# Optimization experiments

Hardware: AMD Instinct MI355X
Metric: run time of the kernel (lower is better)

The kernel has to match this reference:

```python
import jax, jax.numpy as jnp
import numpy as np

N_NODES = 100000
N_EDGES = 1600000
NFEAT = 256
NHID = 128


def setup_inputs() -> dict:
    key = jax.random.key(0)
    ks = jax.random.split(key, 8)
    x = jax.random.normal(ks[0], (N_NODES, NFEAT), dtype=jnp.float32)
    edge_row = jax.random.randint(ks[1], (N_EDGES,), 0, N_NODES, dtype=jnp.int32)
    edge_col = jax.random.randint(ks[2], (N_EDGES,), 0, N_NODES, dtype=jnp.int32)
    edge_val = jax.random.uniform(ks[3], (N_EDGES,), dtype=jnp.float32)
    # Glorot-ish init for the two GraphConvolution weights
    W1 = jax.random.normal(ks[4], (NFEAT, NHID), dtype=jnp.float32) * (1.0 / np.sqrt(NFEAT))
    b1 = jnp.zeros((NHID,), dtype=jnp.float32)
    W2 = jax.random.normal(ks[5], (NHID, NHID), dtype=jnp.float32) * (1.0 / np.sqrt(NHID))
    b2 = jnp.zeros((NHID,), dtype=jnp.float32)
    return {"x": x, "edge_row": edge_row, "edge_col": edge_col,
            "edge_val": edge_val, "W1": W1, "b1": b1, "W2": W2, "b2": b2}


def _gcn_layer(h, W, b, edge_row, edge_col, edge_val, n_nodes):
    # support = h @ W  (dense transform), then spmm(adj, support) + b
    support = h @ W                              # [N, d_out]
    msgs = edge_val[:, None] * support[edge_col]  # [E, d_out] gather
    agg = jax.ops.segment_sum(msgs, edge_row, num_segments=n_nodes)  # scatter-add
    return agg + b


def reference(x, edge_row, edge_col, edge_val, W1, b1, W2, b2):
    n = x.shape[0]
    # eval mode: dropout is identity
    h = jax.nn.relu(_gcn_layer(x, W1, b1, edge_row, edge_col, edge_val, n))
    for _ in range(4):  # gc2 applied 4 times with shared weights
        h = jax.nn.relu(_gcn_layer(h, W2, b2, edge_row, edge_col, edge_val, n))
    return h
```

## Files before the change

### kernel.cpp

```cpp
#include <hip/hip_runtime.h>

constexpr int NFEAT = 256;
constexpr int NHID  = 128;
constexpr int SCAN_B = 4096;


__global__ void hist_kernel(const int* __restrict__ rows, int* __restrict__ cnt, int n) {
  int i = blockIdx.x * blockDim.x + threadIdx.x;
  if (i < n) atomicAdd(&cnt[rows[i]], 1);
}

__global__ void scan1_kernel(const int* __restrict__ cnt, int* __restrict__ part,
                             int* __restrict__ bsum, int n) {
  __shared__ int tmp[1024];
  int tid = threadIdx.x;
  int base = blockIdx.x * SCAN_B + tid * 4;
  int4 v = make_int4(0, 0, 0, 0);
  if (base + 4 <= n) {
    v = *(const int4*)&cnt[base];
  } else {
    if (base + 0 < n) v.x = cnt[base + 0];
    if (base + 1 < n) v.y = cnt[base + 1];
    if (base + 2 < n) v.z = cnt[base + 2];
    if (base + 3 < n) v.w = cnt[base + 3];
  }
  int s = v.x + v.y + v.z + v.w;
  tmp[tid] = s;
  __syncthreads();
  for (int off = 1; off < 1024; off <<= 1) {
    int t = (tid >= off) ? tmp[tid - off] : 0;
    __syncthreads();
    tmp[tid] += t;
    __syncthreads();
  }
  int excl = tmp[tid] - s;
  if (base + 0 < n) part[base + 0] = excl;
  if (base + 1 < n) part[base + 1] = excl + v.x;
  if (base + 2 < n) part[base + 2] = excl + v.x + v.y;
  if (base + 3 < n) part[base + 3] = excl + v.x + v.y + v.z;
  if (tid == 1023) bsum[blockIdx.x] = tmp[1023];
}

__global__ void scan2_kernel(int* __restrict__ bsum, int nb) {
  if (threadIdx.x == 0 && blockIdx.x == 0) {
    int run = 0;
    for (int i = 0; i < nb; ++i) { int t = bsum[i]; bsum[i] = run; run += t; }
    bsum[nb] = run;
  }
}

__global__ void scan3_kernel(int* __restrict__ row_ptr, const int* __restrict__ bsum,
                             int* __restrict__ cursor, int n, int nb) {
  int i = blockIdx.x * blockDim.x + threadIdx.x;
  if (i < n) {
    int v = row_ptr[i] + bsum[i / SCAN_B];
    row_ptr[i] = v;
    cursor[i]  = v;
  }
  if (i == 0) row_ptr[n] = bsum[nb];
}

__global__ void scatter_kernel(const int* __restrict__ rows, const int* __restrict__ cols,
                               const float* __restrict__ vals, int* __restrict__ cursor,
                               int2* __restrict__ ev_s, int n) {
  int i = blockIdx.x * blockDim.x + threadIdx.x;
  if (i < n) {
    int p = atomicAdd(&cursor[rows[i]], 1);
    ev_s[p] = make_int2(cols[i], __float_as_int(vals[i]));
  }
}


__device__ __forceinline__ void gload16(const float* src, float* dst_lds) {
  __builtin_amdgcn_global_load_lds(
      (const __attribute__((address_space(1))) void*)src,
      (__attribute__((address_space(3))) void*)dst_lds,
      16, 0, 0);
}

template<int K>
__global__ __launch_bounds__(256, 4) void gemm_kernel(const float* __restrict__ A,
                                                      const float* __restrict__ W,
                                                      float* __restrict__ C, int M) {
  __shared__ __align__(16) float As[2][2048];
  __shared__ __align__(16) float Bs[2][2048];
  const int tid  = threadIdx.x;
  const int w    = tid >> 6;
  const int lane = tid & 63;
  const int r8   = tid >> 4;
  const int c8   = tid & 15;
  const int block_row = blockIdx.x * 128;

  float acc[2][2][4][4] = {};

  auto prefetch = [&](int t) {
    const int buf = t & 1;
    const int k0  = t * 16;
    #pragma unroll
    for (int j = 0; j < 2; ++j) {
      int s   = j * 256 + w * 64 + lane;
      int row = s >> 2;
      int q   = (s & 3) ^ ((row >> 2) & 3);
      int grow = block_row + row;
      if (grow >= M) grow = M - 1;
      gload16(A + (size_t)grow * K + k0 + q * 4,
              &As[buf][(j * 256 + w * 64) * 4]);
    }
    #pragma unroll
    for (int j = 0; j < 2; ++j) {
      int s = j * 256 + w * 64 + lane;
      int r = s >> 5, cq = s & 31;
      gload16(W + (size_t)(k0 + r) * 128 + cq * 4,
              &Bs[buf][(j * 256 + w * 64) * 4]);
    }
  };

  constexpr int NT = K / 16;
  prefetch(0);
  for (int t = 0; t < NT; ++t) {
    __syncthreads();
    if (t + 1 < NT) prefetch(t + 1);
    const float* as = As[t & 1];
    const float* bs = Bs[t & 1];
    #pragma unroll
    for (int q = 0; q < 4; ++q) {
      float4 b[4][2];
      #pragma unroll
      for (int j = 0; j < 4; ++j) {
        int kk = q * 4 + j;
        b[j][0] = *(const float4*)&bs[(kk * 32 + c8) * 4];
        b[j][1] = *(const float4*)&bs[(kk * 32 + 16 + c8) * 4];
      }
      #pragma unroll
      for (int rh = 0; rh < 2; ++rh)
        #pragma unroll
        for (int i = 0; i < 4; ++i) {
          int row = rh * 64 + r8 * 4 + i;
          float4 a = *(const float4*)&as[(row * 4 + (q ^ ((row >> 2) & 3))) * 4];
          float av[4] = {a.x, a.y, a.z, a.w};
          #pragma unroll
          for (int j = 0; j < 4; ++j)
            #pragma unroll
            for (int ch = 0; ch < 2; ++ch) {
              acc[rh][ch][i][0] += av[j] * b[j][ch].x;
              acc[rh][ch][i][1] += av[j] * b[j][ch].y;
              acc[rh][ch][i][2] += av[j] * b[j][ch].z;
              acc[rh][ch][i][3] += av[j] * b[j][ch].w;
            }
        }
    }
  }

  #pragma unroll
  for (int rh = 0; rh < 2; ++rh)
    #pragma unroll
    for (int i = 0; i < 4; ++i) {
      int grow = block_row + rh * 64 + r8 * 4 + i;
      if (grow < M) {
        #pragma unroll
        for (int ch = 0; ch < 2; ++ch) {
          float4 v = make_float4(acc[rh][ch][i][0], acc[rh][ch][i][1],
                                 acc[rh][ch][i][2], acc[rh][ch][i][3]);
          *(float4*)&C[(size_t)grow * 128 + ch * 64 + c8 * 4] = v;
        }
      }
    }
}


__global__ void spmm_kernel(const float* __restrict__ support, const int* __restrict__ row_ptr,
                            const int2* __restrict__ ev, const float* __restrict__ bias,
                            float* __restrict__ out, int n_nodes) {
  int row  = blockIdx.x * (blockDim.x >> 6) + (threadIdx.x >> 6);
  int lane = threadIdx.x & 63;
  if (row >= n_nodes) return;
  int beg = row_ptr[row], end = row_ptr[row + 1];
  float ax0 = 0.f, ay0 = 0.f, ax1 = 0.f, ay1 = 0.f;
  for (int chunk = beg; chunk < end; chunk += 64) {
    int idx = chunk + lane;
    int m = min(64, end - chunk);
    int2 ee = (idx < end) ? ev[idx] : make_int2(0, 0);
    int cl = ee.x;
    float vl = __int_as_float(ee.y);
    int e = 0;
    for (; e + 8 <= m; e += 8) {
      int   c0 = __shfl(cl, e + 0), c1 = __shfl(cl, e + 1);
      int   c2 = __shfl(cl, e + 2), c3 = __shfl(cl, e + 3);
      int   c4 = __shfl(cl, e + 4), c5 = __shfl(cl, e + 5);
      int   c6 = __shfl(cl, e + 6), c7 = __shfl(cl, e + 7);
      float v0 = __shfl(vl, e + 0), v1 = __shfl(vl, e + 1);
      float v2 = __shfl(vl, e + 2), v3 = __shfl(vl, e + 3);
      float v4 = __shfl(vl, e + 4), v5 = __shfl(vl, e + 5);
      float v6 = __shfl(vl, e + 6), v7 = __shfl(vl, e + 7);
      float2 s0 = *(const float2*)&support[(size_t)c0 * 128 + lane * 2];
      float2 s1 = *(const float2*)&support[(size_t)c1 * 128 + lane * 2];
      float2 s2 = *(const float2*)&support[(size_t)c2 * 128 + lane * 2];
      float2 s3 = *(const float2*)&support[(size_t)c3 * 128 + lane * 2];
      float2 s4 = *(const float2*)&support[(size_t)c4 * 128 + lane * 2];
      float2 s5 = *(const float2*)&support[(size_t)c5 * 128 + lane * 2];
      float2 s6 = *(const float2*)&support[(size_t)c6 * 128 + lane * 2];
      float2 s7 = *(const float2*)&support[(size_t)c7 * 128 + lane * 2];
      ax0 += v0 * s0.x; ay0 += v0 * s0.y;
      ax1 += v1 * s1.x; ay1 += v1 * s1.y;
      ax0 += v2 * s2.x; ay0 += v2 * s2.y;
      ax1 += v3 * s3.x; ay1 += v3 * s3.y;
      ax0 += v4 * s4.x; ay0 += v4 * s4.y;
      ax1 += v5 * s5.x; ay1 += v5 * s5.y;
      ax0 += v6 * s6.x; ay0 += v6 * s6.y;
      ax1 += v7 * s7.x; ay1 += v7 * s7.y;
    }
    for (; e < m; ++e) {
      int   ce = __shfl(cl, e);
      float ve = __shfl(vl, e);
      float2 s = *(const float2*)&support[(size_t)ce * 128 + lane * 2];
      ax0 += ve * s.x; ay0 += ve * s.y;
    }
  }
  float accx = ax0 + ax1, accy = ay0 + ay1;
  float2 b = *(const float2*)&bias[lane * 2];
  float2 o = make_float2(fmaxf(accx + b.x, 0.f), fmaxf(accy + b.y, 0.f));
  *(float2*)&out[(size_t)row * 128 + lane * 2] = o;
}


extern "C" void kernel_launch(void* const* d_in, const int* in_sizes, int n_in,
                              void* d_out, int out_size, void* d_ws, size_t ws_size,
                              hipStream_t stream) {
  const float* x    = (const float*)d_in[0];
  const int*   erow = (const int*)d_in[1];
  const int*   ecol = (const int*)d_in[2];
  const float* evl  = (const float*)d_in[3];
  const float* W1   = (const float*)d_in[4];
  const float* b1   = (const float*)d_in[5];
  const float* W2   = (const float*)d_in[6];
  const float* b2   = (const float*)d_in[7];
  int n_nodes = in_sizes[0] / NFEAT;
  int n_edges = in_sizes[1];
  float* out = (float*)d_out;

  char* ws = (char*)d_ws;
  size_t off = 0;
  auto alloc = [&](size_t bytes) -> void* {
    void* p = ws + off;
    off += bytes;
    off = (off + 255) & ~(size_t)255;
    return p;
  };
  float* support = (float*)alloc((size_t)n_nodes * NHID * sizeof(float));
  int*   cnt     = (int*)alloc((size_t)n_nodes * sizeof(int));
  int*   row_ptr = (int*)alloc(((size_t)n_nodes + 1) * sizeof(int));
  int*   cursor  = (int*)alloc((size_t)n_nodes * sizeof(int));
  int2*  ev_s    = (int2*)alloc((size_t)n_edges * sizeof(int2));
  int nb = (n_nodes + SCAN_B - 1) / SCAN_B;
  int*   bsum    = (int*)alloc((size_t)(nb + 1) * sizeof(int));

  hipMemsetAsync(cnt, 0, (size_t)n_nodes * sizeof(int), stream);
  hist_kernel<<<(n_edges + 255) / 256, 256, 0, stream>>>(erow, cnt, n_edges);
  scan1_kernel<<<nb, 1024, 0, stream>>>(cnt, row_ptr, bsum, n_nodes);
  scan2_kernel<<<1, 64, 0, stream>>>(bsum, nb);
  scan3_kernel<<<(n_nodes + 255) / 256, 256, 0, stream>>>(row_ptr, bsum, cursor, n_nodes, nb);
  scatter_kernel<<<(n_edges + 255) / 256, 256, 0, stream>>>(erow, ecol, evl, cursor,
                                                            ev_s, n_edges);

  int gblocks = (n_nodes + 127) / 128;
  int sblocks = (n_nodes + 3) / 4;

  gemm_kernel<NFEAT><<<gblocks, 256, 0, stream>>>(x, W1, support, n_nodes);
  spmm_kernel<<<sblocks, 256, 0, stream>>>(support, row_ptr, ev_s, b1, out, n_nodes);

  for (int l = 0; l < 4; ++l) {
    gemm_kernel<NHID><<<gblocks, 256, 0, stream>>>(out, W2, support, n_nodes);
    spmm_kernel<<<sblocks, 256, 0, stream>>>(support, row_ptr, ev_s, b2, out, n_nodes);
  }
}
```

Measured before the change: 1.081 ms.

## Store edge permutation instead of packed sorted edges; reorder GEMM inner loop

The scatter step now writes only a permutation index per edge instead of a packed (col, val) pair. Each SpMM then reads the permutation and gathers col and val from the original unsorted edge arrays. The GEMM inner loop is reordered to load all A values first and then stream B values one k at a time, and the occupancy hint is removed from launch_bounds. This lowers setup writes but adds an indirect random gather of col and val in every one of the five SpMM launches.

```diff
diff --git a/kernel.cpp b/kernel.cpp
--- a/kernel.cpp
+++ b/kernel.cpp
@@ -60,13 +60,12 @@
   if (i == 0) row_ptr[n] = bsum[nb];
 }
 
-__global__ void scatter_kernel(const int* __restrict__ rows, const int* __restrict__ cols,
-                               const float* __restrict__ vals, int* __restrict__ cursor,
-                               int2* __restrict__ ev_s, int n) {
+__global__ void scatter_kernel(const int* __restrict__ rows, int* __restrict__ cursor,
+                               int* __restrict__ perm, int n) {
   int i = blockIdx.x * blockDim.x + threadIdx.x;
   if (i < n) {
     int p = atomicAdd(&cursor[rows[i]], 1);
-    ev_s[p] = make_int2(cols[i], __float_as_int(vals[i]));
+    perm[p] = i;
   }
 }
 
@@ -79,9 +78,9 @@
 }
 
 template<int K>
-__global__ __launch_bounds__(256, 4) void gemm_kernel(const float* __restrict__ A,
-                                                      const float* __restrict__ W,
-                                                      float* __restrict__ C, int M) {
+__global__ __launch_bounds__(256) void gemm_kernel(const float* __restrict__ A,
+                                                   const float* __restrict__ W,
+                                                   float* __restrict__ C, int M) {
   __shared__ __align__(16) float As[2][2048];
   __shared__ __align__(16) float Bs[2][2048];
   const int tid  = threadIdx.x;
@@ -124,30 +123,32 @@
     const float* bs = Bs[t & 1];
     #pragma unroll
     for (int q = 0; q < 4; ++q) {
-      float4 b[4][2];
-      #pragma unroll
-      for (int j = 0; j < 4; ++j) {
-        int kk = q * 4 + j;
-        b[j][0] = *(const float4*)&bs[(kk * 32 + c8) * 4];
-        b[j][1] = *(const float4*)&bs[(kk * 32 + 16 + c8) * 4];
-      }
+      float av[2][4][4];
       #pragma unroll
       for (int rh = 0; rh < 2; ++rh)
         #pragma unroll
         for (int i = 0; i < 4; ++i) {
           int row = rh * 64 + r8 * 4 + i;
           float4 a = *(const float4*)&as[(row * 4 + (q ^ ((row >> 2) & 3))) * 4];
-          float av[4] = {a.x, a.y, a.z, a.w};
+          av[rh][i][0] = a.x; av[rh][i][1] = a.y;
+          av[rh][i][2] = a.z; av[rh][i][3] = a.w;
+        }
+      #pragma unroll
+      for (int j = 0; j < 4; ++j) {
+        int kk = q * 4 + j;
+        float4 b0 = *(const float4*)&bs[(kk * 32 + c8) * 4];
+        float4 b1 = *(const float4*)&bs[(kk * 32 + 16 + c8) * 4];
+        #pragma unroll
+        for (int rh = 0; rh < 2; ++rh)
           #pragma unroll
-          for (int j = 0; j < 4; ++j)
-            #pragma unroll
-            for (int ch = 0; ch < 2; ++ch) {
-              acc[rh][ch][i][0] += av[j] * b[j][ch].x;
-              acc[rh][ch][i][1] += av[j] * b[j][ch].y;
-              acc[rh][ch][i][2] += av[j] * b[j][ch].z;
-              acc[rh][ch][i][3] += av[j] * b[j][ch].w;
-            }
-        }
+          for (int i = 0; i < 4; ++i) {
+            float a = av[rh][i][j];
+            acc[rh][0][i][0] += a * b0.x; acc[rh][0][i][1] += a * b0.y;
+            acc[rh][0][i][2] += a * b0.z; acc[rh][0][i][3] += a * b0.w;
+            acc[rh][1][i][0] += a * b1.x; acc[rh][1][i][1] += a * b1.y;
+            acc[rh][1][i][2] += a * b1.z; acc[rh][1][i][3] += a * b1.w;
+          }
+      }
     }
   }
 
@@ -169,7 +170,8 @@
 
 
 __global__ void spmm_kernel(const float* __restrict__ support, const int* __restrict__ row_ptr,
-                            const int2* __restrict__ ev, const float* __restrict__ bias,
+                            const int* __restrict__ perm, const int* __restrict__ ecol,
+                            const float* __restrict__ evl, const float* __restrict__ bias,
                             float* __restrict__ out, int n_nodes) {
   int row  = blockIdx.x * (blockDim.x >> 6) + (threadIdx.x >> 6);
   int lane = threadIdx.x & 63;
@@ -179,9 +181,9 @@
   for (int chunk = beg; chunk < end; chunk += 64) {
     int idx = chunk + lane;
     int m = min(64, end - chunk);
-    int2 ee = (idx < end) ? ev[idx] : make_int2(0, 0);
-    int cl = ee.x;
-    float vl = __int_as_float(ee.y);
+    int ie = (idx < end) ? perm[idx] : 0;
+    int   cl = ecol[ie];
+    float vl = (idx < end) ? evl[ie] : 0.f;
     int e = 0;
     for (; e + 8 <= m; e += 8) {
       int   c0 = __shfl(cl, e + 0), c1 = __shfl(cl, e + 1);
@@ -250,7 +252,7 @@
   int*   cnt     = (int*)alloc((size_t)n_nodes * sizeof(int));
   int*   row_ptr = (int*)alloc(((size_t)n_nodes + 1) * sizeof(int));
   int*   cursor  = (int*)alloc((size_t)n_nodes * sizeof(int));
-  int2*  ev_s    = (int2*)alloc((size_t)n_edges * sizeof(int2));
+  int*   perm    = (int*)alloc((size_t)n_edges * sizeof(int));
   int nb = (n_nodes + SCAN_B - 1) / SCAN_B;
   int*   bsum    = (int*)alloc((size_t)(nb + 1) * sizeof(int));
 
@@ -259,17 +261,16 @@
   scan1_kernel<<<nb, 1024, 0, stream>>>(cnt, row_ptr, bsum, n_nodes);
   scan2_kernel<<<1, 64, 0, stream>>>(bsum, nb);
   scan3_kernel<<<(n_nodes + 255) / 256, 256, 0, stream>>>(row_ptr, bsum, cursor, n_nodes, nb);
-  scatter_kernel<<<(n_edges + 255) / 256, 256, 0, stream>>>(erow, ecol, evl, cursor,
-                                                            ev_s, n_edges);
+  scatter_kernel<<<(n_edges + 255) / 256, 256, 0, stream>>>(erow, cursor, perm, n_edges);
 
   int gblocks = (n_nodes + 127) / 128;
   int sblocks = (n_nodes + 3) / 4;
 
   gemm_kernel<NFEAT><<<gblocks, 256, 0, stream>>>(x, W1, support, n_nodes);
-  spmm_kernel<<<sblocks, 256, 0, stream>>>(support, row_ptr, ev_s, b1, out, n_nodes);
+  spmm_kernel<<<sblocks, 256, 0, stream>>>(support, row_ptr, perm, ecol, evl, b1, out, n_nodes);
 
   for (int l = 0; l < 4; ++l) {
     gemm_kernel<NHID><<<gblocks, 256, 0, stream>>>(out, W2, support, n_nodes);
-    spmm_kernel<<<sblocks, 256, 0, stream>>>(support, row_ptr, ev_s, b2, out, n_nodes);
-  }
-}
+    spmm_kernel<<<sblocks, 256, 0, stream>>>(support, row_ptr, perm, ecol, evl, b2, out, n_nodes);
+  }
+}
```

New measurement: 1.320 ms. +22.1%, slower.
